# Performance work log

Measured on AMD Instinct MI355X. Metric: run time of the kernel, lower is better.

Reference implementation:

```python
import jax, jax.numpy as jnp
import numpy as np
import math
from functools import lru_cache

# ---------- Clebsch-Gordan machinery (numpy, setup-time only) ----------

def _cg(j1, m1, j2, m2, j, m):
    """Complex-basis CG coefficient via Racah's formula (Condon-Shortley)."""
    if m1 + m2 != m:
        return 0.0
    f = math.factorial
    pre = (2 * j + 1) * f(j1 + j2 - j) * f(j1 - j2 + j) * f(-j1 + j2 + j) / f(j1 + j2 + j + 1)
    pre *= f(j1 + m1) * f(j1 - m1) * f(j2 + m2) * f(j2 - m2) * f(j + m) * f(j - m)
    s = 0.0
    for k in range(0, j1 + j2 - j + 1):
        d = (k, j1 + j2 - j - k, j1 - m1 - k, j2 + m2 - k, j - j2 + m1 + k, j - j1 - m2 + k)
        if min(d) < 0:
            continue
        s += (-1) ** k / (f(d[0]) * f(d[1]) * f(d[2]) * f(d[3]) * f(d[4]) * f(d[5]))
    return math.sqrt(pre) * s


def _csh_to_rsh(j):
    """Unitary complex->real spherical harmonics transform, columns indexed by real m."""
    C = np.zeros((2 * j + 1, 2 * j + 1), dtype=np.complex128)
    s2 = 1.0 / math.sqrt(2.0)
    for m in range(-j, j + 1):
        am = abs(m)
        if m < 0:
            C[j + m, j + m] = 1j * s2
            C[j - m, j + m] = -1j * ((-1) ** am) * s2
        elif m == 0:
            C[j, j] = 1.0
        else:
            C[j - m, j + m] = s2
            C[j + m, j + m] = ((-1) ** am) * s2
    return C


@lru_cache(maxsize=None)
def _rsh_cg(j1, j2, j):
    """Real-basis CG, compactified to rows [m1, m2, m, coeff] over nonzeros."""
    csh = np.zeros((2 * j1 + 1, 2 * j2 + 1, 2 * j + 1), dtype=np.complex128)
    for m1 in range(-j1, j1 + 1):
        for m2 in range(-j2, j2 + 1):
            m = m1 + m2
            if -j <= m <= j:
                csh[j1 + m1, j2 + m2, j + m] = _cg(j1, m1, j2, m2, j, m)
    r = np.einsum('abc,ai,bj,ck->ijk', csh, _csh_to_rsh(j1), _csh_to_rsh(j2), np.conj(_csh_to_rsh(j)))
    r = np.real(r * ((-1j) ** (j1 + j2 + j)))
    m1g, m2g, mg = np.meshgrid(np.arange(-j1, j1 + 1), np.arange(-j2, j2 + 1),
                               np.arange(-j, j + 1), indexing='ij')
    mask = np.abs(r) > 1e-12
    return np.stack([m1g[mask].astype(np.float64), m2g[mask].astype(np.float64),
                     mg[mask].astype(np.float64), r[mask]], axis=0)


def _build_coupler(md1, md2, trunc_in=True):
    """Faithful replay of CGPCoupler._init_params: returns cg_tilde, repids, out_dim."""
    md1 = np.asarray(md1, dtype=np.int64)
    md2 = np.asarray(md2, dtype=np.int64)
    md_in = np.stack([md1, md2], axis=0)                      # [2, 2*(L+1)]
    max_n_out = np.maximum(md1, md2)
    nlp = md_in.shape[1]
    n_irr = np.repeat(np.arange(nlp // 2) * 2 + 1, 2)         # irreps per (l,p) slot
    off_in = np.cumsum(md_in * n_irr[None, :], axis=1)
    off_in = np.concatenate([np.zeros((2, 1), dtype=np.int64), off_in[:, :-1]], axis=1)
    max_l = nlp // 2 - 1
    md_out = np.zeros_like(max_n_out)
    valid = []
    for lout in range(max_l + 1):
        for pout in (1, -1):
            for l1 in range(max_l + 1):
                for l2 in range(max_l + 1):
                    for p1 in (1, -1):
                        for p2 in (1, -1):
                            cp = (-1) ** (lout + l1 + l2)
                            if p1 * p2 * cp != pout:
                                continue
                            if l1 + l2 < lout or abs(l1 - l2) > lout:
                                continue
                            lp1 = 2 * l1 + (1 - p1) // 2
                            lp2 = 2 * l2 + (1 - p2) // 2
                            lpo = 2 * lout + (1 - pout) // 2
                            if trunc_in:
                                if l1 + l2 > max_l:
                                    continue
                                deg = min(md_in[0, lp1], md_in[1, lp2],
                                          max_n_out[2 * (l1 + l2) + (1 - pout) // 2])
                            else:
                                deg = min(md_in[0, lp1], md_in[1, lp2], max_n_out[lpo])
                            md_out[lpo] += deg
                            if deg > 0:
                                valid.append((lpo, lp1, lp2, int(deg)))
    off_out = np.cumsum(md_out * n_irr)
    off_out = np.concatenate([[0], off_out[:-1]]).astype(np.int64)
    cg_l, r1_l, r2_l, ro_l = [], [], [], []
    ns_off, lpo_last = 0, 0
    for lpo, lp1, lp2, deg in valid:
        if lpo > lpo_last:
            ns_off = 0
        l1, l2, lout = lp1 // 2, lp2 // 2, lpo // 2
        src = _rsh_cg(l1, l2, lout)                            # [4, nnz]
        seg = np.repeat(src, deg, axis=1)                      # repeat_interleave along dim=1
        ns = np.tile(np.arange(deg, dtype=np.int64), src.shape[1])
        r1_l.append(off_in[0, lp1] + np.rint(seg[0] + l1).astype(np.int64) * md_in[0, lp1] + ns)
        r2_l.append(off_in[1, lp2] + np.rint(seg[1] + l2).astype(np.int64) * md_in[1, lp2] + ns)
        ro_l.append(off_out[lpo] + np.rint(seg[2] + lout).astype(np.int64) * md_out[lpo] + ns_off + ns)
        cg_l.append(seg[3])
        ns_off += deg
        lpo_last = lpo
    out_dim = int(np.sum(md_out * n_irr))
    return (np.concatenate(cg_l), np.concatenate(r1_l), np.concatenate(r2_l),
            np.concatenate(ro_l), out_dim)


METADATA = [32, 32, 32, 32, 32, 32, 32, 32]   # max_l = 3, 32 channels per (l, parity)
BATCH = 2048


def setup_inputs() -> dict:
    key = jax.random.key(0)
    k1, k2 = jax.random.split(key)
    cg, r1, r2, ro, out_dim = _build_coupler(METADATA, METADATA, trunc_in=True)
    n_irr = np.repeat(np.arange(len(METADATA) // 2) * 2 + 1, 2)
    in_dim = int(np.sum(np.asarray(METADATA) * n_irr))        # 1024
    x1 = jax.random.normal(k1, (BATCH, in_dim), dtype=jnp.float32)
    x2 = jax.random.normal(k2, (BATCH, in_dim), dtype=jnp.float32)
    return {
        "x1": x1,
        "x2": x2,
        "cg_tilde": jnp.asarray(cg, dtype=jnp.float32),
        "repids_in1": jnp.asarray(r1, dtype=jnp.int64) if jax.config.jax_enable_x64 else jnp.asarray(r1, dtype=jnp.int32),
        "repids_in2": jnp.asarray(r2, dtype=jnp.int64) if jax.config.jax_enable_x64 else jnp.asarray(r2, dtype=jnp.int32),
        "repids_out": jnp.asarray(ro, dtype=jnp.int64) if jax.config.jax_enable_x64 else jnp.asarray(ro, dtype=jnp.int32),
        "out_dim": out_dim,
    }


def reference(x1, x2, cg_tilde, repids_in1, repids_in2, repids_out, out_dim):
    # gather along rep dim (last), elementwise multiply with CG coeffs, scatter-add
    out_tilde = x1[:, repids_in1] * x2[:, repids_in2] * cg_tilde[None, :]   # [B, K]
    out = jnp.zeros((x1.shape[0], out_dim), dtype=x1.dtype).at[:, repids_out].add(out_tilde)
    return out
```

## Files before the change

kernel.cpp:

```cpp
#include <hip/hip_runtime.h>


#define IN_DIM 1024
#define ROWS   4
#define NOBCAP 512

__global__ __launch_bounds__(1024) void prep_kernel(
    const int* __restrict__ r1, const int* __restrict__ r2,
    const int* __restrict__ ro, const float* __restrict__ cg,
    int nseg, int nob,
    uint2* __restrict__ qdesc, int* __restrict__ zlist, int* __restrict__ hdr)
{
    __shared__ int cntS[NOBCAP];
    __shared__ int qscan[NOBCAP];
    __shared__ int zscan[NOBCAP];
    __shared__ int qoffS[NOBCAP];
    __shared__ unsigned int flagS[NOBCAP];
    __shared__ int rankS[NOBCAP];

    const int t = threadIdx.x;

    for (int j = t; j < NOBCAP; j += 1024) { cntS[j] = 0; rankS[j] = 0; }
    __syncthreads();

    for (int s = t; s < nseg; s += 1024)
        atomicAdd(&cntS[ro[s << 5] >> 5], 1);
    __syncthreads();

    if (t < NOBCAP) {
        const int c = (t < nob) ? cntS[t] : 0;
        qscan[t] = (t < nob) ? (((c > 0 ? c : 1) + 3) >> 2) : 0;
        zscan[t] = (t < nob && c > 4) ? 1 : 0;
    }
    __syncthreads();
    for (int d = 1; d < NOBCAP; d <<= 1) {
        int vq = 0, vz = 0;
        if (t < NOBCAP && t >= d) { vq = qscan[t - d]; vz = zscan[t - d]; }
        __syncthreads();
        if (t < NOBCAP) { qscan[t] += vq; zscan[t] += vz; }
        __syncthreads();
    }
    if (t < nob) {
        const int c  = cntS[t];
        const int q  = ((c > 0 ? c : 1) + 3) >> 2;
        const int qb = qscan[t] - q;
        qoffS[t] = qb;
        const int sh = (c > 4) ? 1 : 0;
        const unsigned int fl = sh ? 0u : 0x80000000u;
        flagS[t] = fl;
        if (sh) zlist[zscan[t] - 1] = t;
        const unsigned int pd = ((unsigned int)t << 20) | fl;
        for (int j = (qb << 2) + c; j < ((qb + q) << 2); ++j)
            qdesc[j] = make_uint2(pd, 0u);
    }
    if (t == 0) {
        const int tot    = qscan[nob - 1];
        const int totPad = (tot + 7) & ~7;
        for (int j = (tot << 2); j < (totPad << 2); ++j)
            qdesc[j] = make_uint2(0u, 0u);
        hdr[0] = totPad;
        hdr[1] = zscan[nob - 1];
    }
    __syncthreads();

    for (int s = t; s < nseg; s += 1024) {
        const int k  = s << 5;
        const int ob = ro[k] >> 5;
        const int slot = (qoffS[ob] << 2) + atomicAdd(&rankS[ob], 1);
        qdesc[slot] = make_uint2((unsigned int)r1[k] | ((unsigned int)r2[k] << 10)
                                 | ((unsigned int)ob << 20) | flagS[ob],
                                 __float_as_uint(cg[k]));
    }
}

__global__ __launch_bounds__(512) void cgp_main(const float* __restrict__ x1,
    const float* __restrict__ x2, const uint2* __restrict__ qdesc,
    const int* __restrict__ zlist, const int* __restrict__ hdr,
    float* __restrict__ out, int out_dim)
{
    __shared__ float x1s[ROWS * IN_DIM];
    __shared__ float x2s[ROWS * IN_DIM];
    const int r0  = blockIdx.x * ROWS;
    const int tid = threadIdx.x;

    {
        const float4* p1 = reinterpret_cast<const float4*>(x1 + (size_t)r0 * IN_DIM);
        const float4* p2 = reinterpret_cast<const float4*>(x2 + (size_t)r0 * IN_DIM);
        float4* s1 = reinterpret_cast<float4*>(x1s);
        float4* s2 = reinterpret_cast<float4*>(x2s);
        for (int j = tid; j < (ROWS * IN_DIM) >> 2; j += 512) { s1[j] = p1[j]; s2[j] = p2[j]; }
    }
    const int nz = hdr[1];
    for (int i = tid; i < (nz << 5); i += 512) {
        const int ob = zlist[i >> 5];
        const int ch = i & 31;
        float* p = out + (size_t)r0 * out_dim + (ob << 5) + ch;
        p[0] = 0.f; p[out_dim] = 0.f; p[2 * out_dim] = 0.f; p[3 * out_dim] = 0.f;
    }
    __syncthreads();

    const int w  = tid >> 6;
    const int ln = tid & 63;
    const int rr = ln >> 4;
    const int tt = ln & 15;
    const float* xs1 = x1s + rr * IN_DIM + (tt << 1);
    const float* xs2 = x2s + rr * IN_DIM + (tt << 1);
    float* orow = out + (size_t)(r0 + rr) * out_dim + (tt << 1);

    const int nquads = hdr[0];
    const int qpw    = nquads >> 3;
    const uint2* qd  = qdesc + ((size_t)(w * qpw) << 2);

    #pragma unroll 2
    for (int i = 0; i < qpw; ++i, qd += 4) {
        const uint4 A  = *reinterpret_cast<const uint4*>(qd);
        const uint4 Bq = *reinterpret_cast<const uint4*>(qd + 2);
        float sx = 0.f, sy = 0.f;
        {
            const float c = __uint_as_float(A.y);
            const float2 u = *reinterpret_cast<const float2*>(xs1 + (A.x & 1023u));
            const float2 v = *reinterpret_cast<const float2*>(xs2 + ((A.x >> 10) & 1023u));
            sx = fmaf(c, u.x * v.x, sx); sy = fmaf(c, u.y * v.y, sy);
        }
        {
            const float c = __uint_as_float(A.w);
            const float2 u = *reinterpret_cast<const float2*>(xs1 + (A.z & 1023u));
            const float2 v = *reinterpret_cast<const float2*>(xs2 + ((A.z >> 10) & 1023u));
            sx = fmaf(c, u.x * v.x, sx); sy = fmaf(c, u.y * v.y, sy);
        }
        {
            const float c = __uint_as_float(Bq.y);
            const float2 u = *reinterpret_cast<const float2*>(xs1 + (Bq.x & 1023u));
            const float2 v = *reinterpret_cast<const float2*>(xs2 + ((Bq.x >> 10) & 1023u));
            sx = fmaf(c, u.x * v.x, sx); sy = fmaf(c, u.y * v.y, sy);
        }
        {
            const float c = __uint_as_float(Bq.w);
            const float2 u = *reinterpret_cast<const float2*>(xs1 + (Bq.z & 1023u));
            const float2 v = *reinterpret_cast<const float2*>(xs2 + ((Bq.z >> 10) & 1023u));
            sx = fmaf(c, u.x * v.x, sx); sy = fmaf(c, u.y * v.y, sy);
        }
        float* p = orow + (((A.x >> 20) & 511u) << 5);
        if (A.x >> 31) {
            *reinterpret_cast<float2*>(p) = make_float2(sx, sy);
        } else {
            unsafeAtomicAdd(p, sx);
            unsafeAtomicAdd(p + 1, sy);
        }
    }
}

extern "C" void kernel_launch(void* const* d_in, const int* in_sizes, int n_in,
                              void* d_out, int out_size, void* d_ws, size_t ws_size,
                              hipStream_t stream)
{
    const float* x1 = (const float*)d_in[0];
    const float* x2 = (const float*)d_in[1];
    const float* cg = (const float*)d_in[2];
    const int*   r1 = (const int*)d_in[3];
    const int*   r2 = (const int*)d_in[4];
    const int*   ro = (const int*)d_in[5];
    float* out = (float*)d_out;

    const int B       = in_sizes[0] / IN_DIM;
    const int out_dim = out_size / B;
    const int K       = in_sizes[2];
    const int nseg    = K >> 5;
    const int nob     = out_dim >> 5;
    const int qcap    = nob + (nseg >> 2) + 16;

    auto align16 = [](size_t v) { return (v + 15) & ~(size_t)15; };
    char* ws = (char*)d_ws;
    uint2* qdesc = (uint2*)ws;  ws += align16((size_t)qcap * 4 * sizeof(uint2));
    int*   zlist = (int*)ws;    ws += align16((size_t)NOBCAP * sizeof(int));
    int*   hdr   = (int*)ws;

    hipLaunchKernelGGL(prep_kernel, dim3(1), dim3(1024), 0, stream,
                       r1, r2, ro, cg, nseg, nob, qdesc, zlist, hdr);
    hipLaunchKernelGGL(cgp_main, dim3(B / ROWS), dim3(512), 0, stream,
                       x1, x2, qdesc, zlist, hdr, out, out_dim);
}
```

Measured before the change: 32.40 us.

## Split small output blocks into pair descriptors and widen lanes to float4 with 8 rows

Output blocks with two or fewer contributing segments now get a separate pair-descriptor list, so they are no longer padded up to quads of four entries. The quad and pair lists are processed in two loops, with padding entries marked by a skip sentinel. Each lane now handles four channels with float4 shared-memory loads, and each block covers 8 rows with 1024 threads. The prep kernel's block-wide scan is replaced by a wave-shuffle scan over packed counters. The aim is to cut wasted padded work and instruction count, at the cost of doubled shared-memory use per block and fewer blocks in flight.

```diff
diff --git a/kernel.cpp b/kernel.cpp
--- a/kernel.cpp
+++ b/kernel.cpp
@@ -1,82 +1,141 @@
 #include <hip/hip_runtime.h>
 
 
-#define IN_DIM 1024
-#define ROWS   4
-#define NOBCAP 512
+#define IN_DIM  1024
+#define ROWS    8
+#define NOBCAP  512
+#define SKIP_OB 511u
 
 __global__ __launch_bounds__(1024) void prep_kernel(
     const int* __restrict__ r1, const int* __restrict__ r2,
     const int* __restrict__ ro, const float* __restrict__ cg,
     int nseg, int nob,
-    uint2* __restrict__ qdesc, int* __restrict__ zlist, int* __restrict__ hdr)
-{
-    __shared__ int cntS[NOBCAP];
-    __shared__ int qscan[NOBCAP];
-    __shared__ int zscan[NOBCAP];
-    __shared__ int qoffS[NOBCAP];
-    __shared__ unsigned int flagS[NOBCAP];
-    __shared__ int rankS[NOBCAP];
-
+    uint2* __restrict__ qdesc, uint2* __restrict__ ddesc,
+    int* __restrict__ zlist, int* __restrict__ hdr)
+{
+    __shared__ int cntS[NOBCAP], rankS[NOBCAP];
+    __shared__ int qoffS[NOBCAP], doffS[NOBCAP];
+    __shared__ int wsum[8], woff[8];
     const int t = threadIdx.x;
 
-    for (int j = t; j < NOBCAP; j += 1024) { cntS[j] = 0; rankS[j] = 0; }
+    if (t < NOBCAP) { cntS[t] = 0; rankS[t] = 0; }
     __syncthreads();
 
     for (int s = t; s < nseg; s += 1024)
         atomicAdd(&cntS[ro[s << 5] >> 5], 1);
     __syncthreads();
 
+    int c = 0;
+    unsigned int pv = 0;
     if (t < NOBCAP) {
-        const int c = (t < nob) ? cntS[t] : 0;
-        qscan[t] = (t < nob) ? (((c > 0 ? c : 1) + 3) >> 2) : 0;
-        zscan[t] = (t < nob && c > 4) ? 1 : 0;
-    }
-    __syncthreads();
-    for (int d = 1; d < NOBCAP; d <<= 1) {
-        int vq = 0, vz = 0;
-        if (t < NOBCAP && t >= d) { vq = qscan[t - d]; vz = zscan[t - d]; }
-        __syncthreads();
-        if (t < NOBCAP) { qscan[t] += vq; zscan[t] += vz; }
-        __syncthreads();
-    }
-    if (t < nob) {
-        const int c  = cntS[t];
-        const int q  = ((c > 0 ? c : 1) + 3) >> 2;
-        const int qb = qscan[t] - q;
-        qoffS[t] = qb;
-        const int sh = (c > 4) ? 1 : 0;
-        const unsigned int fl = sh ? 0u : 0x80000000u;
-        flagS[t] = fl;
-        if (sh) zlist[zscan[t] - 1] = t;
-        const unsigned int pd = ((unsigned int)t << 20) | fl;
-        for (int j = (qb << 2) + c; j < ((qb + q) << 2); ++j)
-            qdesc[j] = make_uint2(pd, 0u);
-    }
-    if (t == 0) {
-        const int tot    = qscan[nob - 1];
-        const int totPad = (tot + 7) & ~7;
-        for (int j = (tot << 2); j < (totPad << 2); ++j)
-            qdesc[j] = make_uint2(0u, 0u);
-        hdr[0] = totPad;
-        hdr[1] = zscan[nob - 1];
+        c = (t < nob) ? cntS[t] : 0;
+        const int q  = (t < nob && c >= 3) ? ((c + 3) >> 2) : 0;
+        const int df = (t < nob && c <= 2) ? 1 : 0;
+        const int zf = (t < nob && c > 4) ? 1 : 0;
+        pv = ((unsigned int)q << 20) | ((unsigned int)df << 10) | (unsigned int)zf;
+    }
+    const int lane = t & 63;
+    const int wid  = t >> 6;
+    #pragma unroll
+    for (int off = 1; off < 64; off <<= 1) {
+        const unsigned int n = __shfl_up(pv, off, 64);
+        if (lane >= off) pv += n;
+    }
+    if (t < NOBCAP && lane == 63) wsum[wid] = (int)pv;
+    __syncthreads();
+    if (t < 8) {
+        unsigned int v = (unsigned int)wsum[t];
+        const unsigned int self = v;
+        #pragma unroll
+        for (int off = 1; off < 8; off <<= 1) {
+            const unsigned int n = __shfl_up(v, off, 64);
+            if (t >= off) v += n;
+        }
+        woff[t] = (int)(v - self);
+    }
+    __syncthreads();
+
+    if (t < NOBCAP) {
+        const unsigned int incl = pv + (unsigned int)woff[wid];
+        const int qi = (incl >> 20) & 1023;
+        const int di = (incl >> 10) & 1023;
+        const int zi = incl & 1023;
+        if (t < nob) {
+            if (c <= 2) {
+                const int db = di - 1;
+                doffS[t] = db;
+                const unsigned int pd = ((unsigned int)t << 20) | 0x80000000u;
+                for (int j = (db << 1) + c; j < ((db + 1) << 1); ++j)
+                    ddesc[j] = make_uint2(pd, 0u);
+            } else {
+                const int qn = (c + 3) >> 2;
+                const int qb = qi - qn;
+                qoffS[t] = qb;
+                const unsigned int fl = (c > 4) ? 0u : 0x80000000u;
+                if (c > 4) zlist[zi - 1] = t;
+                const unsigned int pd = ((unsigned int)t << 20) | fl;
+                for (int j = (qb << 2) + c; j < ((qb + qn) << 2); ++j)
+                    qdesc[j] = make_uint2(pd, 0u);
+            }
+        }
+        if (t == NOBCAP - 1) {
+            const int nq = qi, nd = di;
+            const int nqPad = (nq + 15) & ~15;
+            const int ndPad = (nd + 31) & ~31;
+            const uint2 dummy = make_uint2(SKIP_OB << 20, 0u);
+            for (int j = (nq << 2); j < (nqPad << 2); ++j) qdesc[j] = dummy;
+            for (int j = (nd << 1); j < (ndPad << 1); ++j) ddesc[j] = dummy;
+            hdr[0] = nqPad; hdr[1] = zi; hdr[2] = ndPad;
+        }
     }
     __syncthreads();
 
     for (int s = t; s < nseg; s += 1024) {
         const int k  = s << 5;
         const int ob = ro[k] >> 5;
-        const int slot = (qoffS[ob] << 2) + atomicAdd(&rankS[ob], 1);
-        qdesc[slot] = make_uint2((unsigned int)r1[k] | ((unsigned int)r2[k] << 10)
-                                 | ((unsigned int)ob << 20) | flagS[ob],
-                                 __float_as_uint(cg[k]));
-    }
-}
-
-__global__ __launch_bounds__(512) void cgp_main(const float* __restrict__ x1,
+        const int cc = cntS[ob];
+        const int rk = atomicAdd(&rankS[ob], 1);
+        const unsigned int fl = (cc > 4) ? 0u : 0x80000000u;
+        const uint2 v = make_uint2((unsigned int)r1[k] | ((unsigned int)r2[k] << 10)
+                                   | ((unsigned int)ob << 20) | fl,
+                                   __float_as_uint(cg[k]));
+        if (cc <= 2) ddesc[(doffS[ob] << 1) + rk] = v;
+        else         qdesc[(qoffS[ob] << 2) + rk] = v;
+    }
+}
+
+__device__ __forceinline__ void accum4(float4& acc, unsigned int dx, unsigned int dc,
+                                       const float* xs1, const float* xs2)
+{
+    const float  c = __uint_as_float(dc);
+    const float4 u = *reinterpret_cast<const float4*>(xs1 + (dx & 1023u));
+    const float4 v = *reinterpret_cast<const float4*>(xs2 + ((dx >> 10) & 1023u));
+    acc.x = fmaf(c, u.x * v.x, acc.x);
+    acc.y = fmaf(c, u.y * v.y, acc.y);
+    acc.z = fmaf(c, u.z * v.z, acc.z);
+    acc.w = fmaf(c, u.w * v.w, acc.w);
+}
+
+__device__ __forceinline__ void terminal(float* orow, unsigned int hx, float4 acc,
+                                         int out_dim)
+{
+    const int ob = (int)((hx >> 20) & 511u);
+    if (ob == (int)SKIP_OB) return;
+    float* p = orow + (ob << 5);
+    if (hx >> 31) {
+        *reinterpret_cast<float4*>(p) = acc;
+    } else {
+        unsafeAtomicAdd(p,     acc.x);
+        unsafeAtomicAdd(p + 1, acc.y);
+        unsafeAtomicAdd(p + 2, acc.z);
+        unsafeAtomicAdd(p + 3, acc.w);
+    }
+}
+
+__global__ __launch_bounds__(1024) void cgp_main(const float* __restrict__ x1,
     const float* __restrict__ x2, const uint2* __restrict__ qdesc,
-    const int* __restrict__ zlist, const int* __restrict__ hdr,
-    float* __restrict__ out, int out_dim)
+    const uint2* __restrict__ ddesc, const int* __restrict__ zlist,
+    const int* __restrict__ hdr, float* __restrict__ out, int out_dim)
 {
     __shared__ float x1s[ROWS * IN_DIM];
     __shared__ float x2s[ROWS * IN_DIM];
@@ -88,64 +147,58 @@
         const float4* p2 = reinterpret_cast<const float4*>(x2 + (size_t)r0 * IN_DIM);
         float4* s1 = reinterpret_cast<float4*>(x1s);
         float4* s2 = reinterpret_cast<float4*>(x2s);
-        for (int j = tid; j < (ROWS * IN_DIM) >> 2; j += 512) { s1[j] = p1[j]; s2[j] = p2[j]; }
+        #pragma unroll
+        for (int j = tid; j < (ROWS * IN_DIM) >> 2; j += 1024) { s1[j] = p1[j]; s2[j] = p2[j]; }
     }
     const int nz = hdr[1];
-    for (int i = tid; i < (nz << 5); i += 512) {
+    for (int i = tid; i < (nz << 5); i += 1024) {
         const int ob = zlist[i >> 5];
         const int ch = i & 31;
         float* p = out + (size_t)r0 * out_dim + (ob << 5) + ch;
-        p[0] = 0.f; p[out_dim] = 0.f; p[2 * out_dim] = 0.f; p[3 * out_dim] = 0.f;
+        #pragma unroll
+        for (int j = 0; j < ROWS; ++j) p[j * out_dim] = 0.f;
     }
     __syncthreads();
 
     const int w  = tid >> 6;
     const int ln = tid & 63;
-    const int rr = ln >> 4;
-    const int tt = ln & 15;
-    const float* xs1 = x1s + rr * IN_DIM + (tt << 1);
-    const float* xs2 = x2s + rr * IN_DIM + (tt << 1);
-    float* orow = out + (size_t)(r0 + rr) * out_dim + (tt << 1);
-
-    const int nquads = hdr[0];
-    const int qpw    = nquads >> 3;
-    const uint2* qd  = qdesc + ((size_t)(w * qpw) << 2);
-
-    #pragma unroll 2
-    for (int i = 0; i < qpw; ++i, qd += 4) {
-        const uint4 A  = *reinterpret_cast<const uint4*>(qd);
-        const uint4 Bq = *reinterpret_cast<const uint4*>(qd + 2);
-        float sx = 0.f, sy = 0.f;
-        {
-            const float c = __uint_as_float(A.y);
-            const float2 u = *reinterpret_cast<const float2*>(xs1 + (A.x & 1023u));
-            const float2 v = *reinterpret_cast<const float2*>(xs2 + ((A.x >> 10) & 1023u));
-            sx = fmaf(c, u.x * v.x, sx); sy = fmaf(c, u.y * v.y, sy);
-        }
-        {
-            const float c = __uint_as_float(A.w);
-            const float2 u = *reinterpret_cast<const float2*>(xs1 + (A.z & 1023u));
-            const float2 v = *reinterpret_cast<const float2*>(xs2 + ((A.z >> 10) & 1023u));
-            sx = fmaf(c, u.x * v.x, sx); sy = fmaf(c, u.y * v.y, sy);
-        }
-        {
-            const float c = __uint_as_float(Bq.y);
-            const float2 u = *reinterpret_cast<const float2*>(xs1 + (Bq.x & 1023u));
-            const float2 v = *reinterpret_cast<const float2*>(xs2 + ((Bq.x >> 10) & 1023u));
-            sx = fmaf(c, u.x * v.x, sx); sy = fmaf(c, u.y * v.y, sy);
-        }
-        {
-            const float c = __uint_as_float(Bq.w);
-            const float2 u = *reinterpret_cast<const float2*>(xs1 + (Bq.z & 1023u));
-            const float2 v = *reinterpret_cast<const float2*>(xs2 + ((Bq.z >> 10) & 1023u));
-            sx = fmaf(c, u.x * v.x, sx); sy = fmaf(c, u.y * v.y, sy);
-        }
-        float* p = orow + (((A.x >> 20) & 511u) << 5);
-        if (A.x >> 31) {
-            *reinterpret_cast<float2*>(p) = make_float2(sx, sy);
-        } else {
-            unsafeAtomicAdd(p, sx);
-            unsafeAtomicAdd(p + 1, sy);
+    const int rr = ln >> 3;
+    const int tt = ln & 7;
+    const float* xs1 = x1s + rr * IN_DIM + (tt << 2);
+    const float* xs2 = x2s + rr * IN_DIM + (tt << 2);
+    float* orow = out + (size_t)(r0 + rr) * out_dim + (tt << 2);
+
+    {
+        const int qpw = hdr[0] >> 4;
+        const uint2* qd = qdesc + ((size_t)(w * qpw) << 2);
+        #pragma unroll 2
+        for (int i = 0; i < qpw; ++i, qd += 4) {
+            const uint4 A  = *reinterpret_cast<const uint4*>(qd);
+            const uint4 Bq = *reinterpret_cast<const uint4*>(qd + 2);
+            float4 acc = make_float4(0.f, 0.f, 0.f, 0.f);
+            accum4(acc, A.x,  A.y,  xs1, xs2);
+            accum4(acc, A.z,  A.w,  xs1, xs2);
+            accum4(acc, Bq.x, Bq.y, xs1, xs2);
+            accum4(acc, Bq.z, Bq.w, xs1, xs2);
+            terminal(orow, A.x, acc, out_dim);
+        }
+    }
+
+    {
+        const int ppw = hdr[2] >> 5;
+        const uint2* dd = ddesc + ((size_t)(w * ppw) << 2);
+        #pragma unroll 2
+        for (int i = 0; i < ppw; ++i, dd += 4) {
+            const uint4 A  = *reinterpret_cast<const uint4*>(dd);
+            const uint4 Bq = *reinterpret_cast<const uint4*>(dd + 2);
+            float4 a0 = make_float4(0.f, 0.f, 0.f, 0.f);
+            float4 a1 = make_float4(0.f, 0.f, 0.f, 0.f);
+            accum4(a0, A.x,  A.y,  xs1, xs2);
+            accum4(a0, A.z,  A.w,  xs1, xs2);
+            accum4(a1, Bq.x, Bq.y, xs1, xs2);
+            accum4(a1, Bq.z, Bq.w, xs1, xs2);
+            terminal(orow, A.x,  a0, out_dim);
+            terminal(orow, Bq.x, a1, out_dim);
         }
     }
 }
@@ -167,16 +220,18 @@
     const int K       = in_sizes[2];
     const int nseg    = K >> 5;
     const int nob     = out_dim >> 5;
-    const int qcap    = nob + (nseg >> 2) + 16;
+    const int qcap    = nob + (nseg >> 2) + 32;
+    const int dcap    = nob + 48;
 
     auto align16 = [](size_t v) { return (v + 15) & ~(size_t)15; };
     char* ws = (char*)d_ws;
     uint2* qdesc = (uint2*)ws;  ws += align16((size_t)qcap * 4 * sizeof(uint2));
+    uint2* ddesc = (uint2*)ws;  ws += align16((size_t)dcap * 2 * sizeof(uint2));
     int*   zlist = (int*)ws;    ws += align16((size_t)NOBCAP * sizeof(int));
     int*   hdr   = (int*)ws;
 
     hipLaunchKernelGGL(prep_kernel, dim3(1), dim3(1024), 0, stream,
-                       r1, r2, ro, cg, nseg, nob, qdesc, zlist, hdr);
-    hipLaunchKernelGGL(cgp_main, dim3(B / ROWS), dim3(512), 0, stream,
-                       x1, x2, qdesc, zlist, hdr, out, out_dim);
-}
+                       r1, r2, ro, cg, nseg, nob, qdesc, ddesc, zlist, hdr);
+    hipLaunchKernelGGL(cgp_main, dim3(B / ROWS), dim3(1024), 0, stream,
+                       x1, x2, qdesc, ddesc, zlist, hdr, out, out_dim);
+}
```

Measured after the change: 28.74 us. -11.3%, faster.
